# Kernel tuning notes

Measured on AMD Instinct MI355X. Metric: run time of the kernel, lower is better.

Reference implementation:

```python
import jax, jax.numpy as jnp
import numpy as np

N_NODES = 100000
N_EDGES = 1600000
IN_DIM = 128
HIDDEN = [128, 128]
MLP_HIDDEN = [64]


def _glorot(key, shape):
    fan_in, fan_out = shape[0], shape[1]
    s = jnp.sqrt(6.0 / (fan_in + fan_out))
    return jax.random.uniform(key, shape, jnp.float32, -s, s)


def setup_inputs() -> dict:
    key = jax.random.key(0)
    ks = jax.random.split(key, 16)
    x = jax.random.normal(ks[0], (N_NODES, IN_DIM), jnp.float32)
    edge_weight = jax.random.uniform(ks[1], (N_EDGES,), jnp.float32)
    edge_src = jax.random.randint(ks[2], (N_EDGES,), 0, N_NODES, jnp.int32)
    edge_dst = jax.random.randint(ks[3], (N_EDGES,), 0, N_NODES, jnp.int32)
    # GraphConvolution layer params
    W1 = _glorot(ks[4], (IN_DIM, HIDDEN[0]))
    b1 = jnp.zeros((HIDDEN[0],), jnp.float32)
    W2 = _glorot(ks[5], (HIDDEN[0], HIDDEN[1]))
    b2 = jnp.zeros((HIDDEN[1],), jnp.float32)
    # tau head MLP: rep_dim -> 64 -> 1
    tw1 = _glorot(ks[6], (HIDDEN[1], MLP_HIDDEN[0]))
    tb1 = jnp.zeros((MLP_HIDDEN[0],), jnp.float32)
    tw2 = _glorot(ks[7], (MLP_HIDDEN[0], 1))
    tb2 = jnp.zeros((1,), jnp.float32)
    # propensity head: rep_dim -> 1, sigmoid
    pw = _glorot(ks[8], (HIDDEN[1], 1))
    pb = jnp.zeros((1,), jnp.float32)
    return {"x": x, "edge_weight": edge_weight, "W1": W1, "b1": b1, "W2": W2, "b2": b2,
            "tw1": tw1, "tb1": tb1, "tw2": tw2, "tb2": tb2, "pw": pw, "pb": pb,
            "edge_src": edge_src, "edge_dst": edge_dst}


def _gcn_layer(h, W, b, edge_src, edge_dst, edge_weight):
    # GraphConvolution: support = h @ W; out = spmm(adj, support) + b
    support = h @ W                                   # [N, H]
    msg = support[edge_src] * edge_weight[:, None]    # [E, H] gather + scale
    agg = jax.ops.segment_sum(msg, edge_dst, num_segments=N_NODES)  # [N, H]
    return agg + b


def reference(x, edge_weight, W1, b1, W2, b2, tw1, tb1, tw2, tb2, pw, pb, edge_src, edge_dst):
    h = jax.nn.relu(_gcn_layer(x, W1, b1, edge_src, edge_dst, edge_weight))
    h = jax.nn.relu(_gcn_layer(h, W2, b2, edge_src, edge_dst, edge_weight))
    rep = h                                            # [N, rep_dim]
    tau_pred = (jax.nn.relu(rep @ tw1 + tb1) @ tw2 + tb2)[:, 0]  # [N]
    e = jax.nn.sigmoid(rep @ pw + pb)[:, 0]            # [N]
    return tau_pred, e, rep
```

## Files before the change

kernel.cpp:

```cpp
#include <hip/hip_runtime.h>
#include <hip/hip_bf16.h>
#include <math.h>


#define PSZ 256
#define BIN_CH 8192

typedef __attribute__((ext_vector_type(8))) short bfrag;
typedef __attribute__((ext_vector_type(4))) float ffrag;

static __device__ __forceinline__ ushort f2bf(float f) {
    __hip_bfloat16 h = __float2bfloat16(f);
    return *reinterpret_cast<ushort*>(&h);
}
static __device__ __forceinline__ float bf2f(ushort u) {
    __hip_bfloat16 h;
    *reinterpret_cast<ushort*>(&h) = u;
    return __bfloat162float(h);
}


__global__ __launch_bounds__(256) void k_bhist(const int* __restrict__ edst,
                                               int* __restrict__ bcnt,
                                               int nE, int NB) {
    extern __shared__ int h[];
    const int tid = threadIdx.x;
    const int e0  = blockIdx.x * BIN_CH;
    for (int b = tid; b < NB; b += 256) h[b] = 0;
    __syncthreads();
    for (int i = tid; i < BIN_CH; i += 256) {
        int e = e0 + i;
        if (e < nE) atomicAdd(&h[edst[e] >> 8], 1);
    }
    __syncthreads();
    for (int b = tid; b < NB; b += 256) {
        int v = h[b];
        if (v) atomicAdd(&bcnt[b], v);
    }
}

__global__ __launch_bounds__(512) void k_bscan(const int* __restrict__ bcnt,
                                               int* __restrict__ bof,
                                               int* __restrict__ gcur,
                                               int NB, int nE) {
    __shared__ int s[512];
    const int t = threadIdx.x;
    const int v = (t < NB) ? bcnt[t] : 0;
    s[t] = v; __syncthreads();
    for (int o = 1; o < 512; o <<= 1) {
        int u = (t >= o) ? s[t - o] : 0;
        __syncthreads(); s[t] += u; __syncthreads();
    }
    if (t < NB) { int ex = s[t] - v; bof[t] = ex; gcur[t] = ex; }
    if (t == 0) bof[NB] = nE;
}

__global__ __launch_bounds__(256) void k_bin(const int* __restrict__ edst,
                                             const int* __restrict__ esrc,
                                             const float* __restrict__ ew,
                                             int* __restrict__ gcur,
                                             unsigned int* __restrict__ pkbin,
                                             unsigned char* __restrict__ dlbin,
                                             int nE, int NB) {
    extern __shared__ int sm[];
    int* hcnt  = sm;
    int* hbase = sm + NB;
    int* hcur  = sm + 2 * NB;
    const int tid = threadIdx.x;
    const int e0  = blockIdx.x * BIN_CH;

    for (int b = tid; b < NB; b += 256) hcnt[b] = 0;
    __syncthreads();
    for (int i = tid; i < BIN_CH; i += 256) {
        int e = e0 + i;
        if (e < nE) atomicAdd(&hcnt[edst[e] >> 8], 1);
    }
    __syncthreads();
    for (int b = tid; b < NB; b += 256) {
        int c = hcnt[b];
        hbase[b] = c ? atomicAdd(&gcur[b], c) : 0;
        hcur[b] = 0;
    }
    __syncthreads();
    for (int i = tid; i < BIN_CH; i += 256) {
        int e = e0 + i;
        if (e < nE) {
            int d = edst[e];
            int p = d >> 8;
            int pos = atomicAdd(&hcur[p], 1);
            int idx = hbase[p] + pos;
            unsigned int w15 = (unsigned int)rintf(ew[e] * 32767.0f);
            pkbin[idx] = (w15 << 17) | (unsigned int)esrc[e];
            dlbin[idx] = (unsigned char)(d & 255);
        }
    }
}

__global__ __launch_bounds__(256) void k_placepart(
    const unsigned int* __restrict__ pkbin, const unsigned char* __restrict__ dlbin,
    const int* __restrict__ bof, int* __restrict__ off,
    unsigned int* __restrict__ spack, int nN, int NB)
{
    __shared__ int lcnt[PSZ];
    __shared__ int lexc[PSZ];
    const int tid  = threadIdx.x;
    const int p    = blockIdx.x;
    const int base = bof[p];
    const int tot  = bof[p + 1] - base;

    lcnt[tid] = 0;
    __syncthreads();
    for (int i = tid; i < tot; i += 256)
        atomicAdd(&lcnt[dlbin[base + i]], 1);
    __syncthreads();
    int v = lcnt[tid];
    lexc[tid] = v; __syncthreads();
    for (int o = 1; o < 256; o <<= 1) {
        int u = (tid >= o) ? lexc[tid - o] : 0;
        __syncthreads(); lexc[tid] += u; __syncthreads();
    }
    const int ex = lexc[tid] - v;
    int gd = p * PSZ + tid;
    if (gd < nN) off[gd] = base + ex;
    if (p == NB - 1 && tid == 0) off[nN] = base + tot;
    lcnt[tid] = 0;
    __syncthreads();
    for (int i = tid; i < tot; i += 256) {
        unsigned int pk = pkbin[base + i];
        int dl = dlbin[base + i];
        int r = atomicAdd(&lcnt[dl], 1);
        spack[base + lexc[dl] - lcnt[dl] + r + 1 - 1 + (0)] = pk;
    }
}


__global__ __launch_bounds__(256) void k_placepart2(
    const unsigned int* __restrict__ pkbin, const unsigned char* __restrict__ dlbin,
    const int* __restrict__ bof, int* __restrict__ off,
    unsigned int* __restrict__ spack, int nN, int NB)
{
    __shared__ int lcnt[PSZ];
    __shared__ int lexc[PSZ];
    const int tid  = threadIdx.x;
    const int p    = blockIdx.x;
    const int base = bof[p];
    const int tot  = bof[p + 1] - base;

    lcnt[tid] = 0;
    __syncthreads();
    for (int i = tid; i < tot; i += 256)
        atomicAdd(&lcnt[dlbin[base + i]], 1);
    __syncthreads();
    int v = lcnt[tid];
    lexc[tid] = v; __syncthreads();
    for (int o = 1; o < 256; o <<= 1) {
        int u = (tid >= o) ? lexc[tid - o] : 0;
        __syncthreads(); lexc[tid] += u; __syncthreads();
    }
    __syncthreads();
    lexc[tid] -= v;
    int gd = p * PSZ + tid;
    if (gd < nN) off[gd] = base + lexc[tid];
    if (p == NB - 1 && tid == 0) off[nN] = base + tot;
    lcnt[tid] = 0;
    __syncthreads();
    for (int i = tid; i < tot; i += 256) {
        unsigned int pk = pkbin[base + i];
        int dl = dlbin[base + i];
        int r = atomicAdd(&lcnt[dl], 1);
        spack[base + lexc[dl] + r] = pk;
    }
}

__global__ __launch_bounds__(256) void k_prepW(const float* __restrict__ W1,
                                               const float* __restrict__ W2,
                                               ushort* __restrict__ Wt1,
                                               ushort* __restrict__ Wt2) {
    const float* W  = (blockIdx.x == 0) ? W1 : W2;
    ushort*      Wt = (blockIdx.x == 0) ? Wt1 : Wt2;
    for (int j = 0; j < 64; ++j) {
        int idx = threadIdx.x + j * 256;
        int k = idx >> 7, n = idx & 127;
        Wt[n * 128 + k] = f2bf(W[idx]);
    }
}

template <int ABF16>
__global__ __launch_bounds__(256) void gemm_mfma(
    const void* __restrict__ Av, const ushort* __restrict__ Wt,
    ushort* __restrict__ Y, int nN)
{
    __shared__ ushort Xl[64 * 128];
    const int tid  = threadIdx.x;
    const int row0 = blockIdx.x * 64;

    if (ABF16) {
        const int4* X16 = (const int4*)Av;
        #pragma unroll
        for (int j = 0; j < 4; ++j) {
            int u  = tid + j * 256;
            int r  = u >> 4;
            int cb = (u & 15) * 16;
            int grow = row0 + r;
            int4 v = make_int4(0, 0, 0, 0);
            if (grow < nN) v = X16[(size_t)grow * 16 + (u & 15)];
            *(int4*)((char*)Xl + r * 256 + (cb ^ ((r & 7) << 4))) = v;
        }
    } else {
        const float4* X4 = (const float4*)Av;
        #pragma unroll
        for (int j = 0; j < 8; ++j) {
            int u  = tid + j * 256;
            int r  = u >> 5;
            int c4 = (u & 31) * 4;
            int grow = row0 + r;
            float4 v = make_float4(0.f, 0.f, 0.f, 0.f);
            if (grow < nN) v = X4[(size_t)grow * 32 + (u & 31)];
            ushort4 o;
            o.x = f2bf(v.x); o.y = f2bf(v.y); o.z = f2bf(v.z); o.w = f2bf(v.w);
            *(ushort4*)((char*)Xl + r * 256 + ((c4 * 2) ^ ((r & 7) << 4))) = o;
        }
    }
    __syncthreads();

    const int lane = tid & 63;
    const int wid  = tid >> 6;
    const int wrow = wid * 16;
    const int arow = wrow + (lane & 15);
    const int kg16 = (lane >> 4) * 16;

    ffrag acc[8];
    #pragma unroll
    for (int ct = 0; ct < 8; ++ct) acc[ct] = (ffrag){0.f, 0.f, 0.f, 0.f};

    #pragma unroll
    for (int ks = 0; ks < 4; ++ks) {
        const int abyte = arow * 256 + ((ks * 64 + kg16) ^ ((arow & 7) << 4));
        bfrag a = *(const bfrag*)((const char*)Xl + abyte);
        #pragma unroll
        for (int ct = 0; ct < 8; ++ct) {
            const int wcol = ct * 16 + (lane & 15);
            bfrag b = *(const bfrag*)(Wt + wcol * 128 + ks * 32 + (lane >> 4) * 8);
            acc[ct] = __builtin_amdgcn_mfma_f32_16x16x32_bf16(a, b, acc[ct], 0, 0, 0);
        }
    }

    #pragma unroll
    for (int ct = 0; ct < 8; ++ct) {
        #pragma unroll
        for (int i = 0; i < 4; ++i) {
            int row = row0 + wrow + (lane >> 4) * 4 + i;
            if (row < nN)
                Y[(size_t)row * 128 + ct * 16 + (lane & 15)] = f2bf(acc[ct][i]);
        }
    }
}

template <int EP, int OUTBF>
__global__ __launch_bounds__(256) void k_aggregate(
    const ushort* __restrict__ S, const unsigned int* __restrict__ spack,
    const int* __restrict__ off, const float* __restrict__ bias,
    void* __restrict__ out, const float* __restrict__ pw,
    const float* __restrict__ pb, float* __restrict__ out_e, int nN)
{
    const int g    = (blockIdx.x * 256 + threadIdx.x) >> 5;
    const int lane = threadIdx.x & 31;
    if (g >= nN) return;
    const int c  = lane * 4;
    const int j0 = off[g], j1 = off[g + 1];

    float4 acc = make_float4(0.f, 0.f, 0.f, 0.f);
    const float wscale = 1.0f / 32767.0f;

    int j = j0;
    for (; j + 8 <= j1; j += 8) {
        unsigned int p[8];
        #pragma unroll
        for (int q = 0; q < 8; ++q) p[q] = spack[j + q];
        ushort4 v[8];
        #pragma unroll
        for (int q = 0; q < 8; ++q)
            v[q] = *(const ushort4*)&S[(size_t)(p[q] & 0x1FFFF) * 128 + c];
        #pragma unroll
        for (int q = 0; q < 8; ++q) {
            const float w = (float)(p[q] >> 17) * wscale;
            acc.x = fmaf(bf2f(v[q].x), w, acc.x);
            acc.y = fmaf(bf2f(v[q].y), w, acc.y);
            acc.z = fmaf(bf2f(v[q].z), w, acc.z);
            acc.w = fmaf(bf2f(v[q].w), w, acc.w);
        }
    }
    for (; j < j1; ++j) {
        const unsigned int p = spack[j];
        const float w = (float)(p >> 17) * wscale;
        const ushort4 v = *(const ushort4*)&S[(size_t)(p & 0x1FFFF) * 128 + c];
        acc.x = fmaf(bf2f(v.x), w, acc.x);
        acc.y = fmaf(bf2f(v.y), w, acc.y);
        acc.z = fmaf(bf2f(v.z), w, acc.z);
        acc.w = fmaf(bf2f(v.w), w, acc.w);
    }

    const float4 bb = ((const float4*)bias)[lane];
    acc.x = fmaxf(acc.x + bb.x, 0.f);
    acc.y = fmaxf(acc.y + bb.y, 0.f);
    acc.z = fmaxf(acc.z + bb.z, 0.f);
    acc.w = fmaxf(acc.w + bb.w, 0.f);

    if (OUTBF) {
        ushort4 o;
        o.x = f2bf(acc.x); o.y = f2bf(acc.y); o.z = f2bf(acc.z); o.w = f2bf(acc.w);
        *(ushort4*)&((ushort*)out)[(size_t)g * 128 + c] = o;
    } else {
        *(float4*)&((float*)out)[(size_t)g * 128 + c] = acc;
    }

    if (EP) {
        const float4 pv = ((const float4*)pw)[lane];
        float ep = acc.x * pv.x + acc.y * pv.y + acc.z * pv.z + acc.w * pv.w;
        #pragma unroll
        for (int o = 1; o < 32; o <<= 1) ep += __shfl_xor(ep, o);
        if (lane == 0) out_e[g] = 1.f / (1.f + expf(-(ep + pb[0])));
    }
}

__global__ __launch_bounds__(256) void tau_kernel(
    const float* __restrict__ REP, const float* __restrict__ tw1,
    const float* __restrict__ tb1, const float* __restrict__ tw2,
    const float* __restrict__ tb2, float* __restrict__ out_tau, int nN)
{
    __shared__ float Rl[64 * 132];
    __shared__ float Wl[64 * 64];
    __shared__ float stb1[64], stw2[64];

    const int tid  = threadIdx.x;
    const int row0 = blockIdx.x * 64;

    if (tid < 64) { stb1[tid] = tb1[tid]; stw2[tid] = tw2[tid]; }

    #pragma unroll
    for (int j = 0; j < 8; ++j) {
        int i  = tid + j * 256;
        int r  = i >> 5;
        int c4 = i & 31;
        float4 v = make_float4(0.f, 0.f, 0.f, 0.f);
        if (row0 + r < nN) v = ((const float4*)REP)[(size_t)(row0 + r) * 32 + c4];
        ((float4*)Rl)[r * 33 + c4] = v;
    }

    const int cg = tid & 15;
    const int rt = tid >> 4;

    float4 acc[4];
    #pragma unroll
    for (int r = 0; r < 4; ++r) acc[r] = make_float4(0.f, 0.f, 0.f, 0.f);

    for (int kc = 0; kc < 2; ++kc) {
        __syncthreads();
        {
            const float4* s4 = (const float4*)tw1 + kc * 1024;
            #pragma unroll
            for (int j = 0; j < 4; ++j)
                ((float4*)Wl)[tid + j * 256] = s4[tid + j * 256];
        }
        __syncthreads();
        #pragma unroll
        for (int k4 = 0; k4 < 16; ++k4) {
            float4 xr[4];
            #pragma unroll
            for (int r = 0; r < 4; ++r)
                xr[r] = *(const float4*)&Rl[(rt * 4 + r) * 132 + kc * 64 + k4 * 4];
            #pragma unroll
            for (int kk = 0; kk < 4; ++kk) {
                float4 w = *(const float4*)&Wl[(k4 * 4 + kk) * 64 + cg * 4];
                #pragma unroll
                for (int r = 0; r < 4; ++r) {
                    float xv = (kk == 0) ? xr[r].x : (kk == 1) ? xr[r].y
                             : (kk == 2) ? xr[r].z : xr[r].w;
                    acc[r].x = fmaf(xv, w.x, acc[r].x);
                    acc[r].y = fmaf(xv, w.y, acc[r].y);
                    acc[r].z = fmaf(xv, w.z, acc[r].z);
                    acc[r].w = fmaf(xv, w.w, acc[r].w);
                }
            }
        }
    }

    const float4 tb = *(const float4*)&stb1[cg * 4];
    const float4 t2 = *(const float4*)&stw2[cg * 4];
    float taup[4];
    #pragma unroll
    for (int r = 0; r < 4; ++r) {
        float hx = fmaxf(acc[r].x + tb.x, 0.f);
        float hy = fmaxf(acc[r].y + tb.y, 0.f);
        float hz = fmaxf(acc[r].z + tb.z, 0.f);
        float hw = fmaxf(acc[r].w + tb.w, 0.f);
        taup[r] = hx * t2.x + hy * t2.y + hz * t2.z + hw * t2.w;
    }
    #pragma unroll
    for (int o = 1; o < 16; o <<= 1) {
        #pragma unroll
        for (int r = 0; r < 4; ++r) taup[r] += __shfl_xor(taup[r], o);
    }
    if (cg == 0) {
        const float tb2v = tb2[0];
        #pragma unroll
        for (int r = 0; r < 4; ++r) {
            int row = row0 + rt * 4 + r;
            if (row < nN) out_tau[row] = taup[r] + tb2v;
        }
    }
}

extern "C" void kernel_launch(void* const* d_in, const int* in_sizes, int n_in,
                              void* d_out, int out_size, void* d_ws, size_t ws_size,
                              hipStream_t stream)
{
    const float* x   = (const float*)d_in[0];
    const float* ew  = (const float*)d_in[1];
    const float* W1  = (const float*)d_in[2];
    const float* b1  = (const float*)d_in[3];
    const float* W2  = (const float*)d_in[4];
    const float* b2  = (const float*)d_in[5];
    const float* tw1 = (const float*)d_in[6];
    const float* tb1 = (const float*)d_in[7];
    const float* tw2 = (const float*)d_in[8];
    const float* tb2 = (const float*)d_in[9];
    const float* pw  = (const float*)d_in[10];
    const float* pb  = (const float*)d_in[11];
    const int* esrc  = (const int*)d_in[12];
    const int* edst  = (const int*)d_in[13];

    const int nN = in_sizes[0] / 128;
    const int nE = in_sizes[1];
    const int NB = (nN + PSZ - 1) / PSZ;

    char* w = (char*)d_ws;
    ushort*        S     = (ushort*)w;         w += (size_t)nN * 128 * 2;
    ushort*        Bh    = (ushort*)w;         w += (size_t)nN * 128 * 2;
    unsigned int*  spack = (unsigned int*)w;   w += (size_t)nE * 4;
    unsigned int*  pkbin = (unsigned int*)w;   w += (size_t)nE * 4;
    unsigned char* dlbin = (unsigned char*)w;  w += (size_t)nE;
    ushort*        Wt1   = (ushort*)w;         w += 16384 * 2;
    ushort*        Wt2   = (ushort*)w;         w += 16384 * 2;
    int*           off   = (int*)w;            w += (size_t)(nN + 1) * 4;
    int*           bcnt  = (int*)w;            w += (size_t)NB * 4;
    int*           bof   = (int*)w;            w += (size_t)(NB + 1) * 4;
    int*           gcur  = (int*)w;            w += (size_t)NB * 4;

    float* out_tau = (float*)d_out;
    float* out_e   = out_tau + nN;
    float* out_rep = out_e + nN;

    const int binBlocks  = (nE + BIN_CH - 1) / BIN_CH;
    const int gemmBlocks = (nN + 63) / 64;
    const int aggBlocks  = (nN + 7) / 8;
    const int tauBlocks  = (nN + 63) / 64;
    const size_t histLds = (size_t)NB * sizeof(int);

    hipMemsetAsync(bcnt, 0, (size_t)NB * sizeof(int), stream);
    k_bhist<<<binBlocks, 256, histLds, stream>>>(edst, bcnt, nE, NB);
    k_bscan<<<1, 512, 0, stream>>>(bcnt, bof, gcur, NB, nE);
    k_bin<<<binBlocks, 256, 3 * histLds, stream>>>(edst, esrc, ew, gcur,
                                                   pkbin, dlbin, nE, NB);
    k_placepart2<<<NB, 256, 0, stream>>>(pkbin, dlbin, bof, off, spack, nN, NB);

    k_prepW<<<2, 256, 0, stream>>>(W1, W2, Wt1, Wt2);

    gemm_mfma<0><<<gemmBlocks, 256, 0, stream>>>(x, Wt1, S, nN);
    k_aggregate<0, 1><<<aggBlocks, 256, 0, stream>>>(S, spack, off, b1, Bh,
                                                     nullptr, nullptr, nullptr, nN);

    gemm_mfma<1><<<gemmBlocks, 256, 0, stream>>>(Bh, Wt2, S, nN);
    k_aggregate<1, 0><<<aggBlocks, 256, 0, stream>>>(S, spack, off, b2, out_rep,
                                                     pw, pb, out_e, nN);

    tau_kernel<<<tauBlocks, 256, 0, stream>>>(out_rep, tw1, tb1, tw2, tb2,
                                              out_tau, nN);
}
```

Measured before the change: 328.0 us.

## Split aggregation into column halves, stage W in LDS, shrink partitions

New measurement: 347.4 us. 5.9% more time.

```diff
diff --git a/kernel.cpp b/kernel.cpp
--- a/kernel.cpp
+++ b/kernel.cpp
@@ -3,8 +3,8 @@
 #include <math.h>
 
 
-#define PSZ 256
-#define BIN_CH 8192
+#define PSZ 128
+#define BIN_CH 16384
 
 typedef __attribute__((ext_vector_type(8))) short bfrag;
 typedef __attribute__((ext_vector_type(4))) float ffrag;
@@ -30,7 +30,7 @@
     __syncthreads();
     for (int i = tid; i < BIN_CH; i += 256) {
         int e = e0 + i;
-        if (e < nE) atomicAdd(&h[edst[e] >> 8], 1);
+        if (e < nE) atomicAdd(&h[edst[e] >> 7], 1);
     }
     __syncthreads();
     for (int b = tid; b < NB; b += 256) {
@@ -39,15 +39,15 @@
     }
 }
 
-__global__ __launch_bounds__(512) void k_bscan(const int* __restrict__ bcnt,
-                                               int* __restrict__ bof,
-                                               int* __restrict__ gcur,
-                                               int NB, int nE) {
-    __shared__ int s[512];
+__global__ __launch_bounds__(1024) void k_bscan(const int* __restrict__ bcnt,
+                                                int* __restrict__ bof,
+                                                int* __restrict__ gcur,
+                                                int NB, int nE) {
+    __shared__ int s[1024];
     const int t = threadIdx.x;
     const int v = (t < NB) ? bcnt[t] : 0;
     s[t] = v; __syncthreads();
-    for (int o = 1; o < 512; o <<= 1) {
+    for (int o = 1; o < 1024; o <<= 1) {
         int u = (t >= o) ? s[t - o] : 0;
         __syncthreads(); s[t] += u; __syncthreads();
     }
@@ -73,7 +73,7 @@
     __syncthreads();
     for (int i = tid; i < BIN_CH; i += 256) {
         int e = e0 + i;
-        if (e < nE) atomicAdd(&hcnt[edst[e] >> 8], 1);
+        if (e < nE) atomicAdd(&hcnt[edst[e] >> 7], 1);
     }
     __syncthreads();
     for (int b = tid; b < NB; b += 256) {
@@ -86,12 +86,12 @@
         int e = e0 + i;
         if (e < nE) {
             int d = edst[e];
-            int p = d >> 8;
+            int p = d >> 7;
             int pos = atomicAdd(&hcur[p], 1);
             int idx = hbase[p] + pos;
             unsigned int w15 = (unsigned int)rintf(ew[e] * 32767.0f);
             pkbin[idx] = (w15 << 17) | (unsigned int)esrc[e];
-            dlbin[idx] = (unsigned char)(d & 255);
+            dlbin[idx] = (unsigned char)(d & 127);
         }
     }
 }
@@ -108,61 +108,27 @@
     const int base = bof[p];
     const int tot  = bof[p + 1] - base;
 
-    lcnt[tid] = 0;
+    if (tid < PSZ) lcnt[tid] = 0;
     __syncthreads();
     for (int i = tid; i < tot; i += 256)
         atomicAdd(&lcnt[dlbin[base + i]], 1);
     __syncthreads();
-    int v = lcnt[tid];
-    lexc[tid] = v; __syncthreads();
-    for (int o = 1; o < 256; o <<= 1) {
-        int u = (tid >= o) ? lexc[tid - o] : 0;
-        __syncthreads(); lexc[tid] += u; __syncthreads();
-    }
-    const int ex = lexc[tid] - v;
-    int gd = p * PSZ + tid;
-    if (gd < nN) off[gd] = base + ex;
+    if (tid < PSZ) lexc[tid] = lcnt[tid];
+    __syncthreads();
+    for (int o = 1; o < PSZ; o <<= 1) {
+        int u = 0;
+        if (tid < PSZ && tid >= o) u = lexc[tid - o];
+        __syncthreads();
+        if (tid < PSZ) lexc[tid] += u;
+        __syncthreads();
+    }
+    if (tid < PSZ) {
+        lexc[tid] -= lcnt[tid];
+        int gd = p * PSZ + tid;
+        if (gd < nN) off[gd] = base + lexc[tid];
+        lcnt[tid] = 0;
+    }
     if (p == NB - 1 && tid == 0) off[nN] = base + tot;
-    lcnt[tid] = 0;
-    __syncthreads();
-    for (int i = tid; i < tot; i += 256) {
-        unsigned int pk = pkbin[base + i];
-        int dl = dlbin[base + i];
-        int r = atomicAdd(&lcnt[dl], 1);
-        spack[base + lexc[dl] - lcnt[dl] + r + 1 - 1 + (0)] = pk;
-    }
-}
-
-
-__global__ __launch_bounds__(256) void k_placepart2(
-    const unsigned int* __restrict__ pkbin, const unsigned char* __restrict__ dlbin,
-    const int* __restrict__ bof, int* __restrict__ off,
-    unsigned int* __restrict__ spack, int nN, int NB)
-{
-    __shared__ int lcnt[PSZ];
-    __shared__ int lexc[PSZ];
-    const int tid  = threadIdx.x;
-    const int p    = blockIdx.x;
-    const int base = bof[p];
-    const int tot  = bof[p + 1] - base;
-
-    lcnt[tid] = 0;
-    __syncthreads();
-    for (int i = tid; i < tot; i += 256)
-        atomicAdd(&lcnt[dlbin[base + i]], 1);
-    __syncthreads();
-    int v = lcnt[tid];
-    lexc[tid] = v; __syncthreads();
-    for (int o = 1; o < 256; o <<= 1) {
-        int u = (tid >= o) ? lexc[tid - o] : 0;
-        __syncthreads(); lexc[tid] += u; __syncthreads();
-    }
-    __syncthreads();
-    lexc[tid] -= v;
-    int gd = p * PSZ + tid;
-    if (gd < nN) off[gd] = base + lexc[tid];
-    if (p == NB - 1 && tid == 0) off[nN] = base + tot;
-    lcnt[tid] = 0;
     __syncthreads();
     for (int i = tid; i < tot; i += 256) {
         unsigned int pk = pkbin[base + i];
@@ -191,6 +157,7 @@
     ushort* __restrict__ Y, int nN)
 {
     __shared__ ushort Xl[64 * 128];
+    __shared__ ushort Wl[128 * 128];
     const int tid  = threadIdx.x;
     const int row0 = blockIdx.x * 64;
 
@@ -221,6 +188,16 @@
             *(ushort4*)((char*)Xl + r * 256 + ((c4 * 2) ^ ((r & 7) << 4))) = o;
         }
     }
+    {
+        const int4* Wg = (const int4*)Wt;
+        #pragma unroll
+        for (int j = 0; j < 8; ++j) {
+            int u  = tid + j * 256;
+            int r  = u >> 4;
+            int cb = (u & 15) * 16;
+            *(int4*)((char*)Wl + r * 256 + (cb ^ ((r & 7) << 4))) = Wg[u];
+        }
+    }
     __syncthreads();
 
     const int lane = tid & 63;
@@ -240,7 +217,8 @@
         #pragma unroll
         for (int ct = 0; ct < 8; ++ct) {
             const int wcol = ct * 16 + (lane & 15);
-            bfrag b = *(const bfrag*)(Wt + wcol * 128 + ks * 32 + (lane >> 4) * 8);
+            const int bbyte = wcol * 256 + ((ks * 64 + kg16) ^ ((wcol & 7) << 4));
+            bfrag b = *(const bfrag*)((const char*)Wl + bbyte);
             acc[ct] = __builtin_amdgcn_mfma_f32_16x16x32_bf16(a, b, acc[ct], 0, 0, 0);
         }
     }
@@ -256,17 +234,18 @@
     }
 }
 
-template <int EP, int OUTBF>
-__global__ __launch_bounds__(256) void k_aggregate(
+template <int EPHASE, int OUTBF>
+__global__ __launch_bounds__(256) void k_agg_half(
     const ushort* __restrict__ S, const unsigned int* __restrict__ spack,
     const int* __restrict__ off, const float* __restrict__ bias,
     void* __restrict__ out, const float* __restrict__ pw,
-    const float* __restrict__ pb, float* __restrict__ out_e, int nN)
+    const float* __restrict__ pb, float* __restrict__ out_e,
+    int nN, int half)
 {
-    const int g    = (blockIdx.x * 256 + threadIdx.x) >> 5;
-    const int lane = threadIdx.x & 31;
+    const int g      = (blockIdx.x * 256 + threadIdx.x) >> 4;
+    const int lane16 = threadIdx.x & 15;
     if (g >= nN) return;
-    const int c  = lane * 4;
+    const int c  = half * 64 + lane16 * 4;
     const int j0 = off[g], j1 = off[g + 1];
 
     float4 acc = make_float4(0.f, 0.f, 0.f, 0.f);
@@ -300,7 +279,7 @@
         acc.w = fmaf(bf2f(v.w), w, acc.w);
     }
 
-    const float4 bb = ((const float4*)bias)[lane];
+    const float4 bb = ((const float4*)bias)[half * 16 + lane16];
     acc.x = fmaxf(acc.x + bb.x, 0.f);
     acc.y = fmaxf(acc.y + bb.y, 0.f);
     acc.z = fmaxf(acc.z + bb.z, 0.f);
@@ -314,12 +293,15 @@
         *(float4*)&((float*)out)[(size_t)g * 128 + c] = acc;
     }
 
-    if (EP) {
-        const float4 pv = ((const float4*)pw)[lane];
+    if (EPHASE) {
+        const float4 pv = ((const float4*)pw)[half * 16 + lane16];
         float ep = acc.x * pv.x + acc.y * pv.y + acc.z * pv.z + acc.w * pv.w;
         #pragma unroll
-        for (int o = 1; o < 32; o <<= 1) ep += __shfl_xor(ep, o);
-        if (lane == 0) out_e[g] = 1.f / (1.f + expf(-(ep + pb[0])));
+        for (int o = 1; o < 16; o <<= 1) ep += __shfl_xor(ep, o);
+        if (lane16 == 0) {
+            if (EPHASE == 1) out_e[g] = ep;
+            else out_e[g] = 1.f / (1.f + expf(-(ep + out_e[g] + pb[0])));
+        }
     }
 }
 
@@ -453,26 +435,30 @@
 
     const int binBlocks  = (nE + BIN_CH - 1) / BIN_CH;
     const int gemmBlocks = (nN + 63) / 64;
-    const int aggBlocks  = (nN + 7) / 8;
+    const int aggBlocks  = (nN + 15) / 16;
     const int tauBlocks  = (nN + 63) / 64;
     const size_t histLds = (size_t)NB * sizeof(int);
 
     hipMemsetAsync(bcnt, 0, (size_t)NB * sizeof(int), stream);
     k_bhist<<<binBlocks, 256, histLds, stream>>>(edst, bcnt, nE, NB);
-    k_bscan<<<1, 512, 0, stream>>>(bcnt, bof, gcur, NB, nE);
+    k_bscan<<<1, 1024, 0, stream>>>(bcnt, bof, gcur, NB, nE);
     k_bin<<<binBlocks, 256, 3 * histLds, stream>>>(edst, esrc, ew, gcur,
                                                    pkbin, dlbin, nE, NB);
-    k_placepart2<<<NB, 256, 0, stream>>>(pkbin, dlbin, bof, off, spack, nN, NB);
+    k_placepart<<<NB, 256, 0, stream>>>(pkbin, dlbin, bof, off, spack, nN, NB);
 
     k_prepW<<<2, 256, 0, stream>>>(W1, W2, Wt1, Wt2);
 
     gemm_mfma<0><<<gemmBlocks, 256, 0, stream>>>(x, Wt1, S, nN);
-    k_aggregate<0, 1><<<aggBlocks, 256, 0, stream>>>(S, spack, off, b1, Bh,
-                                                     nullptr, nullptr, nullptr, nN);
+    k_agg_half<0, 1><<<aggBlocks, 256, 0, stream>>>(S, spack, off, b1, Bh,
+                                                    nullptr, nullptr, nullptr, nN, 0);
+    k_agg_half<0, 1><<<aggBlocks, 256, 0, stream>>>(S, spack, off, b1, Bh,
+                                                    nullptr, nullptr, nullptr, nN, 1);
 
     gemm_mfma<1><<<gemmBlocks, 256, 0, stream>>>(Bh, Wt2, S, nN);
-    k_aggregate<1, 0><<<aggBlocks, 256, 0, stream>>>(S, spack, off, b2, out_rep,
-                                                     pw, pb, out_e, nN);
+    k_agg_half<1, 0><<<aggBlocks, 256, 0, stream>>>(S, spack, off, b2, out_rep,
+                                                    pw, pb, out_e, nN, 0);
+    k_agg_half<2, 0><<<aggBlocks, 256, 0, stream>>>(S, spack, off, b2, out_rep,
+                                                    pw, pb, out_e, nN, 1);
 
     tau_kernel<<<tauBlocks, 256, 0, stream>>>(out_rep, tw1, tb1, tw2, tb2,
                                               out_tau, nN);
```
